# Optimization experiments

Measured on AMD Instinct MI355X. Metric: run time of the kernel, lower is better.

Reference implementation:

```python
import jax, jax.numpy as jnp
import numpy as np

DN = ('NCHW', 'OIHW', 'NCHW')


def conv2d(x, w, pad, dil):
    return jax.lax.conv_general_dilated(x, w, (1, 1), [(pad, pad), (pad, pad)],
                                        rhs_dilation=(dil, dil), dimension_numbers=DN)


def group_norm(x, scale, bias, groups=16, eps=1e-5):
    B, C, H, W = x.shape
    xg = x.reshape(B, groups, -1)
    mu = xg.mean(-1, keepdims=True)
    var = xg.var(-1, keepdims=True)
    xg = (xg - mu) / jnp.sqrt(var + eps)
    return xg.reshape(B, C, H, W) * scale[None, :, None, None] + bias[None, :, None, None]


def aspp_block(x, w, s, b, pad, dil):
    return jax.nn.relu(group_norm(conv2d(x, w, pad, dil), s, b))


def cc_module(q, k, v):
    # criss-cross attention with channel-cosine-normalized q/k
    eps = 1e-10
    qn = q / (jnp.sqrt(jnp.sum(q * q, axis=1, keepdims=True)) + eps)  # norm over channel
    kn = k / (jnp.sqrt(jnp.sum(k * k, axis=1, keepdims=True)) + eps)
    H = q.shape[2]
    # energy along column (vary h') and row (vary w')
    eH = jnp.einsum('bchw,bcgw->bhwg', qn, kn)  # [B,H,W,H]
    eW = jnp.einsum('bchw,bchv->bhwv', qn, kn)  # [B,H,W,W]
    att = jax.nn.softmax(jnp.concatenate([eH, eW], axis=-1), axis=-1)
    attH, attW = att[..., :H], att[..., H:]
    outH = jnp.einsum('bcgw,bhwg->bchw', v, attH)
    outW = jnp.einsum('bchv,bhwv->bchw', v, attW)
    return outH + outW


def cam_module(x, gamma):
    # channel attention with spatial-cosine-normalized similarity
    B, C, H, W = x.shape
    f = x.reshape(B, C, H * W)
    fn = f / (jnp.sqrt(jnp.sum(f * f, axis=-1, keepdims=True)) + 1e-10)
    energy = jnp.einsum('bcn,bdn->bcd', fn, fn)  # [B,C,C]
    att = jax.nn.softmax(energy, axis=-1)
    out = jnp.einsum('bcd,bdn->bcn', att, f).reshape(B, C, H, W)
    return gamma * out + x


def setup_inputs() -> dict:
    key = jax.random.key(0)
    ks = jax.random.split(key, 32)
    C, Cq = 256, 64
    d = {}
    d['x'] = jax.random.normal(ks[0], (4, C, 128, 128), dtype=jnp.float32)
    d['w1'] = jax.random.normal(ks[1], (C, C, 1, 1), jnp.float32) * 0.05
    d['w2'] = jax.random.normal(ks[2], (C, C, 3, 3), jnp.float32) * 0.02
    d['w3'] = jax.random.normal(ks[3], (C, C, 3, 3), jnp.float32) * 0.02
    d['w4'] = jax.random.normal(ks[4], (C, C, 3, 3), jnp.float32) * 0.02
    d['wc'] = jax.random.normal(ks[5], (C, C, 3, 3), jnp.float32) * 0.02
    for i, nm in enumerate(['s1', 's2', 's3', 's4', 'sc']):
        d[nm] = jnp.ones((C,), jnp.float32)
    for nm in ['b1', 'b2', 'b3', 'b4', 'bc']:
        d[nm] = jnp.zeros((C,), jnp.float32)
    d['wq'] = jax.random.normal(ks[6], (Cq, C, 1, 1), jnp.float32) * 0.05
    d['bq'] = jnp.zeros((Cq,), jnp.float32)
    d['wk'] = jax.random.normal(ks[7], (Cq, C, 1, 1), jnp.float32) * 0.05
    d['bk'] = jnp.zeros((Cq,), jnp.float32)
    d['wv'] = jax.random.normal(ks[8], (C, C, 1, 1), jnp.float32) * 0.05
    d['bv'] = jnp.zeros((C,), jnp.float32)
    d['gammas'] = jax.random.normal(ks[9], (5,), jnp.float32) * 0.1
    return d


def reference(x, w1, w2, w3, w4, wc, s1, s2, s3, s4, sc, b1, b2, b3, b4, bc,
              wq, bq, wk, bk, wv, bv, gammas):
    dil = (1, 6, 12, 18)
    x1 = aspp_block(x, w1, s1, b1, pad=0, dil=dil[0])
    x2 = aspp_block(x, w2, s2, b2, pad=dil[1], dil=dil[1])
    x3 = aspp_block(x, w3, s3, b3, pad=dil[2], dil=dil[2])
    x4 = aspp_block(x, w4, s4, b4, pad=dil[3], dil=dil[3])
    x5 = aspp_block(x, wc, sc, bc, pad=1, dil=1)
    for _ in range(2):
        q = conv2d(x5, wq, 0, 1) + bq[None, :, None, None]
        k = conv2d(x5, wk, 0, 1) + bk[None, :, None, None]
        v = conv2d(x5, wv, 0, 1) + bv[None, :, None, None]
        x5 = cc_module(q, k, v)
    L = [x1, x2, x3, x4, x5]
    L = [cam_module(L[i], gammas[i]) for i in range(5)]
    return jnp.stack(L)  # [5, B, C, H, W]
```

## Files before the change

### kernel.cpp

```cpp
#include <hip/hip_runtime.h>
#include <hip/hip_bf16.h>

typedef __hip_bfloat16 bf16;
typedef unsigned short u16;
typedef __attribute__((ext_vector_type(8))) short short8v;
typedef __attribute__((ext_vector_type(4))) float f32x4;

#define BB   4
#define CC_  256
#define HH   128
#define WW   128
#define HWn  16384
#define SZ   ((size_t)16777216)

__device__ __forceinline__ float b2f(bf16 v){ return __bfloat162float(v); }
__device__ __forceinline__ bf16  f2b(float v){ return __float2bfloat16(v); }
__device__ __forceinline__ float us2f(u16 u){
  union { unsigned int i; float f; } x; x.i = ((unsigned int)u) << 16; return x.f;
}
__device__ __forceinline__ u16 f2us(float v){
  bf16 h = f2b(v); u16 u; __builtin_memcpy(&u, &h, 2); return u;
}
__device__ __forceinline__ void st4(float* p, float a, float b, float c, float d){
  *(float4*)p = make_float4(a,b,c,d);
}
__device__ __forceinline__ void st4(bf16* p, float a, float b, float c, float d){
  bf16 o[4] = { f2b(a), f2b(b), f2b(c), f2b(d) };
  *(uint2*)p = *(uint2*)o;
}
__device__ __forceinline__ void store1(float* p, float v){ *p = v; }
__device__ __forceinline__ void store1(bf16* p, float v){ *p = f2b(v); }

typedef __attribute__((address_space(1))) const unsigned int u32g;
typedef __attribute__((address_space(3))) unsigned int u32l;
__device__ __forceinline__ void gl16(const void* g, void* l)
{
  u32g* gp = (u32g*)(unsigned long long)(size_t)g;
  u32l* lp = (u32l*)(unsigned int)(size_t)l;
  __builtin_amdgcn_global_load_lds(gp, lp, 16, 0, 0);
}

__global__ __launch_bounds__(256)
void k_xpose(const float* __restrict__ x, bf16* __restrict__ xt)
{
  const int b = blockIdx.x >> 7, h = blockIdx.x & 127;
  __shared__ u16 L[64][132];
  const int tid = threadIdx.x;
  for (int c0 = 0; c0 < 256; c0 += 64) {
    for (int idx = tid; idx < 2048; idx += 256) {
      const int c = idx >> 5, w4 = (idx & 31) * 4;
      const float4 v = *(const float4*)&x[(((size_t)(b*CC_ + c0 + c))*HH + h)*WW + w4];
      L[c][w4]   = f2us(v.x); L[c][w4+1] = f2us(v.y);
      L[c][w4+2] = f2us(v.z); L[c][w4+3] = f2us(v.w);
    }
    __syncthreads();
    for (int idx = tid; idx < 1024; idx += 256) {
      const int w = idx >> 3, cg = (idx & 7) * 8;
      u16 tmp[8];
      #pragma unroll
      for (int j = 0; j < 8; ++j) tmp[j] = L[cg + j][w];
      *(uint4*)&xt[(((size_t)(b*HH + h))*WW + w)*256 + c0 + cg] = *(uint4*)tmp;
    }
    __syncthreads();
  }
}

__global__ __launch_bounds__(256)
void k_xposeb(const bf16* __restrict__ xt, float* __restrict__ x)
{
  const int b = blockIdx.x >> 7, h = blockIdx.x & 127;
  __shared__ u16 L[64][132];
  const int tid = threadIdx.x;
  for (int c0 = 0; c0 < 256; c0 += 64) {
    for (int idx = tid; idx < 1024; idx += 256) {
      const int w = idx >> 3, cg = (idx & 7) * 8;
      u16 t[8];
      *(uint4*)t = *(const uint4*)((const u16*)xt + (((size_t)(b*HH + h))*WW + w)*256 + c0 + cg);
      #pragma unroll
      for (int j = 0; j < 8; ++j) L[cg + j][w] = t[j];
    }
    __syncthreads();
    for (int idx = tid; idx < 2048; idx += 256) {
      const int c = idx >> 5, w4 = (idx & 31) * 4;
      st4(&x[(((size_t)(b*CC_ + c0 + c))*HH + h)*WW + w4],
          us2f(L[c][w4]), us2f(L[c][w4+1]), us2f(L[c][w4+2]), us2f(L[c][w4+3]));
    }
    __syncthreads();
  }
}

__global__ __launch_bounds__(256)
void k_wt(const float* __restrict__ w, bf16* __restrict__ wt, int taps)
{
  const int i = blockIdx.x * 256 + threadIdx.x;
  const int tap = i >> 16, r = i & 65535;
  const int co = r >> 8, ci = r & 255;
  if (tap < taps) wt[i] = f2b(w[(co*256 + ci)*taps + tap]);
}

template<int KHW, typename DT, bool TRANS>
__global__ __launch_bounds__(256)
void k_convm(const bf16* __restrict__ xt, const bf16* __restrict__ wt,
             const float* __restrict__ bias, DT* __restrict__ dst, int dil, int CO)
{
  const int b   = blockIdx.y >> 7;
  const int h   = blockIdx.y & 127;
  const int co0 = blockIdx.x * 64;
  const int tid = threadIdx.x;
  const int wid = tid >> 6;
  const int lane = tid & 63;
  const int lr = lane & 15;
  const int lg = lane >> 4;
  const int lrow = lane >> 2;
  const int lci  = (lane & 3) * 8;

  __shared__ __align__(16) u16 Asld[KHW*64][32];
  __shared__ __align__(16) u16 Bsld[164][32];

  for (int i = tid; i < 36*32; i += 256) {
    int r = i >> 5; r = (r < 18) ? r : (128 + r);
    Bsld[r][i & 31] = 0;
  }

  f32x4 acc[4][2] = {};

  for (int kh = 0; kh < KHW; ++kh) {
    const int hh = h + (kh - (KHW >> 1)) * dil;
    if (hh < 0 || hh >= HH) continue;
    const bf16* __restrict__ brow = xt + ((size_t)(b*HH + hh))*WW*256;
    for (int kc = 0; kc < 256; kc += 32) {
      for (int ch = wid; ch < KHW*4; ch += 4) {
        const int row = ch*16 + lrow;
        const int tap = row >> 6, cc = row & 63;
        gl16(wt + ((size_t)(kh*KHW + tap))*CO*256 + (co0 + cc)*256 + kc + lci,
             &Asld[ch*16][0]);
      }
      for (int ch = wid; ch < 8; ch += 4) {
        const int wpos = ch*16 + lrow;
        gl16(brow + (size_t)wpos*256 + kc + lci, &Bsld[18 + ch*16][0]);
      }
      __syncthreads();
      #pragma unroll
      for (int kw = 0; kw < KHW; ++kw) {
        const int pbase = 18 + (kw - (KHW >> 1)) * dil;
        short8v af[4], bfr[2];
        #pragma unroll
        for (int cf = 0; cf < 4; ++cf)
          af[cf] = *(const short8v*)&Asld[kw*64 + cf*16 + lr][lg*8];
        #pragma unroll
        for (int wf = 0; wf < 2; ++wf)
          bfr[wf] = *(const short8v*)&Bsld[pbase + wid*32 + wf*16 + lr][lg*8];
        #pragma unroll
        for (int cf = 0; cf < 4; ++cf)
          #pragma unroll
          for (int wf = 0; wf < 2; ++wf)
            acc[cf][wf] = __builtin_amdgcn_mfma_f32_16x16x32_bf16(
                            af[cf], bfr[wf], acc[cf][wf], 0, 0, 0);
      }
      __syncthreads();
    }
  }
  if constexpr (TRANS) {
    #pragma unroll
    for (int cf = 0; cf < 4; ++cf) {
      float bb[4];
      #pragma unroll
      for (int r = 0; r < 4; ++r)
        bb[r] = bias ? bias[co0 + cf*16 + lg*4 + r] : 0.f;
      #pragma unroll
      for (int wf = 0; wf < 2; ++wf) {
        const int wpix = wid*32 + wf*16 + lr;
        bf16* dr = (bf16*)dst + (((size_t)(b*HH + h))*WW + wpix)*CO + co0 + cf*16 + lg*4;
        bf16 o4[4];
        #pragma unroll
        for (int r = 0; r < 4; ++r) o4[r] = f2b(acc[cf][wf][r] + bb[r]);
        *(uint2*)dr = *(uint2*)o4;
      }
    }
  } else {
    #pragma unroll
    for (int cf = 0; cf < 4; ++cf) {
      #pragma unroll
      for (int r = 0; r < 4; ++r) {
        const int co = co0 + cf*16 + lg*4 + r;
        const float bb = bias ? bias[co] : 0.f;
        DT* drow = dst + (((size_t)(b*CO + co))*HH + h)*WW;
        #pragma unroll
        for (int wf = 0; wf < 2; ++wf)
          store1(drow + wid*32 + wf*16 + lr, acc[cf][wf][r] + bb);
      }
    }
  }
}

__global__ __launch_bounds__(256)
void k_gn_stats16(const bf16* __restrict__ t, float* __restrict__ stats)
{
  const int blk = blockIdx.x;
  const int s = blk & 15, bg = blk >> 4;
  const int b = bg >> 4, g = bg & 15;
  const u16* __restrict__ base = (const u16*)t + ((size_t)(b*CC_ + g*16))*HWn + s*1024;
  float s0 = 0.f, s1 = 0.f;
  for (int c = 0; c < 16; ++c) {
    const ushort4 u = *(const ushort4*)(base + (size_t)c * HWn + threadIdx.x*4);
    const float v0 = us2f(u.x), v1 = us2f(u.y), v2 = us2f(u.z), v3 = us2f(u.w);
    s0 += v0 + v1 + v2 + v3;
    s1 = fmaf(v0,v0, fmaf(v1,v1, fmaf(v2,v2, fmaf(v3,v3, s1))));
  }
  #pragma unroll
  for (int o = 32; o > 0; o >>= 1) { s0 += __shfl_down(s0, o, 64); s1 += __shfl_down(s1, o, 64); }
  __shared__ float sh[8];
  const int wid = threadIdx.x >> 6, lane = threadIdx.x & 63;
  if (lane == 0) { sh[wid*2] = s0; sh[wid*2+1] = s1; }
  __syncthreads();
  if (threadIdx.x == 0) {
    atomicAdd(&stats[bg*2],   sh[0]+sh[2]+sh[4]+sh[6]);
    atomicAdd(&stats[bg*2+1], sh[1]+sh[3]+sh[5]+sh[7]);
  }
}

__global__ __launch_bounds__(256)
void k_gn_apply16(const bf16* __restrict__ t, const float* __restrict__ stats,
                  const float* __restrict__ sc, const float* __restrict__ bi,
                  float* __restrict__ dst)
{
  const size_t e = ((size_t)blockIdx.x * 256 + threadIdx.x) * 4;
  const int c  = (int)((e >> 14) & 255);
  const int bg = (int)(e >> 22) * 16 + (c >> 4);
  const float cnt = 16.f * 16384.f;
  const float mu  = stats[bg*2] / cnt;
  const float var = stats[bg*2+1] / cnt - mu * mu;
  const float rs  = rsqrtf(var + 1e-5f);
  const float a   = rs * sc[c];
  const float bb  = bi[c] - mu * a;
  const ushort4 u = *(const ushort4*)((const u16*)t + e);
  st4(dst + e, fmaxf(us2f(u.x)*a+bb,0.f), fmaxf(us2f(u.y)*a+bb,0.f),
               fmaxf(us2f(u.z)*a+bb,0.f), fmaxf(us2f(u.w)*a+bb,0.f));
}

__global__ __launch_bounds__(256)
void k_gn_applyb(const bf16* __restrict__ t, const float* __restrict__ stats,
                 const float* __restrict__ sc, const float* __restrict__ bi,
                 bf16* __restrict__ dst)
{
  const size_t e = ((size_t)blockIdx.x * 256 + threadIdx.x) * 4;
  const int c  = (int)((e >> 14) & 255);
  const int bg = (int)(e >> 22) * 16 + (c >> 4);
  const float cnt = 16.f * 16384.f;
  const float mu  = stats[bg*2] / cnt;
  const float var = stats[bg*2+1] / cnt - mu * mu;
  const float rs  = rsqrtf(var + 1e-5f);
  const float a   = rs * sc[c];
  const float bb  = bi[c] - mu * a;
  const ushort4 u = *(const ushort4*)((const u16*)t + e);
  st4(dst + e, fmaxf(us2f(u.x)*a+bb,0.f), fmaxf(us2f(u.y)*a+bb,0.f),
               fmaxf(us2f(u.z)*a+bb,0.f), fmaxf(us2f(u.w)*a+bb,0.f));
}

__global__ __launch_bounds__(256)
void k_energym(const bf16* __restrict__ fb, float* __restrict__ energy)
{
  const int b  = blockIdx.z;
  const int c0 = (blockIdx.x >> 1) * 128, d0 = (blockIdx.x & 1) * 128;
  const int k0 = blockIdx.y * 512;
  __shared__ __align__(16) u16 Au[2][128][32];
  __shared__ __align__(16) u16 Bu[2][128][32];
  const int tid = threadIdx.x;
  const int wid = tid >> 6, lane = tid & 63;
  const int lr = lane & 15, lg = lane >> 4;
  const int lrow = lane >> 2, lci = (lane & 3) * 8;
  const int row0w = (wid & 1) * 64, col0w = (wid >> 1) * 64;
  const u16* __restrict__ fbb = (const u16*)fb + (size_t)b * CC_ * HWn;

  f32x4 acc[4][4] = {};

  for (int kc = 0; kc < 512; kc += 64) {
    for (int ci = wid; ci < 16; ci += 4) {
      const int seg = ci >> 3, rq = (ci & 7) * 16;
      const int m = rq + lrow;
      gl16(fbb + (size_t)(c0 + m)*HWn + k0 + kc + seg*32 + lci, &Au[seg][rq][0]);
      gl16(fbb + (size_t)(d0 + m)*HWn + k0 + kc + seg*32 + lci, &Bu[seg][rq][0]);
    }
    __syncthreads();
    #pragma unroll
    for (int ks = 0; ks < 2; ++ks) {
      short8v af[4], bfv[4];
      #pragma unroll
      for (int cf = 0; cf < 4; ++cf)
        af[cf] = *(const short8v*)&Au[ks][row0w + cf*16 + lr][lg*8];
      #pragma unroll
      for (int df = 0; df < 4; ++df)
        bfv[df] = *(const short8v*)&Bu[ks][col0w + df*16 + lr][lg*8];
      #pragma unroll
      for (int cf = 0; cf < 4; ++cf)
        #pragma unroll
        for (int df = 0; df < 4; ++df)
          acc[cf][df] = __builtin_amdgcn_mfma_f32_16x16x32_bf16(
                          af[cf], bfv[df], acc[cf][df], 0, 0, 0);
    }
    __syncthreads();
  }
  #pragma unroll
  for (int cf = 0; cf < 4; ++cf)
    #pragma unroll
    for (int df = 0; df < 4; ++df)
      #pragma unroll
      for (int r = 0; r < 4; ++r) {
        const int row = c0 + row0w + cf*16 + lg*4 + r;
        const int col = d0 + col0w + df*16 + lr;
        atomicAdd(&energy[((size_t)(b*CC_ + row))*CC_ + col], acc[cf][df][r]);
      }
}

__global__ __launch_bounds__(512)
void k_camoutm(const float* __restrict__ catt, const bf16* __restrict__ fb,
               float* __restrict__ fio, const float* __restrict__ gammas, int gi)
{
  const int b  = blockIdx.y;
  const int n0 = blockIdx.x * 128;
  __shared__ u16 Au[256][40];
  __shared__ u16 Bu[128][40];
  const int tid = threadIdx.x;
  const int wid = tid >> 6, lane = tid & 63;
  const int lr = lane & 15, lg = lane >> 4;
  const int row0w = (wid & 3) * 64, col0w = (wid >> 2) * 64;

  f32x4 acc[4][4] = {};

  for (int k0 = 0; k0 < 256; k0 += 32) {
    {
      const int m = tid >> 1, kh = (tid & 1) * 16;
      const float* src = catt + ((size_t)(b*CC_ + m))*CC_ + k0 + kh;
      u16 t[16];
      #pragma unroll
      for (int j = 0; j < 4; ++j) {
        const float4 v = *(const float4*)(src + j*4);
        t[j*4]=f2us(v.x); t[j*4+1]=f2us(v.y); t[j*4+2]=f2us(v.z); t[j*4+3]=f2us(v.w);
      }
      *(uint4*)&Au[m][kh]   = *(uint4*)&t[0];
      *(uint4*)&Au[m][kh+8] = *(uint4*)&t[8];
    }
    {
      const int kk = tid >> 4, cl = tid & 15;
      const u16* src = (const u16*)fb + ((size_t)(b*CC_ + k0 + kk))*HWn + n0 + cl;
      #pragma unroll
      for (int j = 0; j < 8; ++j)
        Bu[cl + 16*j][kk] = src[16*j];
    }
    __syncthreads();
    short8v af[4], bfv[4];
    #pragma unroll
    for (int cf = 0; cf < 4; ++cf)
      af[cf] = *(const short8v*)&Au[row0w + cf*16 + lr][lg*8];
    #pragma unroll
    for (int df = 0; df < 4; ++df)
      bfv[df] = *(const short8v*)&Bu[col0w + df*16 + lr][lg*8];
    #pragma unroll
    for (int cf = 0; cf < 4; ++cf)
      #pragma unroll
      for (int df = 0; df < 4; ++df)
        acc[cf][df] = __builtin_amdgcn_mfma_f32_16x16x32_bf16(
                        af[cf], bfv[df], acc[cf][df], 0, 0, 0);
    __syncthreads();
  }
  const float g = gammas[gi];
  #pragma unroll
  for (int cf = 0; cf < 4; ++cf)
    #pragma unroll
    for (int df = 0; df < 4; ++df)
      #pragma unroll
      for (int r = 0; r < 4; ++r) {
        const int row = row0w + cf*16 + lg*4 + r;
        const int col = n0 + col0w + df*16 + lr;
        const size_t o = ((size_t)(b*CC_ + row))*HWn + col;
        fio[o] = g*acc[cf][df][r] + us2f(((const u16*)fb)[o]);
      }
}

__global__ __launch_bounds__(256)
void k_qknorm_t(bf16* __restrict__ q)
{
  const int pix = blockIdx.x * 256 + threadIdx.x;
  u16* __restrict__ base = (u16*)q + (size_t)pix * 64;
  u16 t[64];
  #pragma unroll
  for (int j = 0; j < 8; ++j) *(uint4*)&t[j*8] = *(const uint4*)(base + j*8);
  float s = 0.f;
  #pragma unroll
  for (int c = 0; c < 64; ++c) { const float v = us2f(t[c]); s = fmaf(v, v, s); }
  const float rn = 1.f / (sqrtf(s) + 1e-10f);
  #pragma unroll
  for (int c = 0; c < 64; ++c) t[c] = f2us(us2f(t[c]) * rn);
  #pragma unroll
  for (int j = 0; j < 8; ++j) *(uint4*)(base + j*8) = *(uint4*)&t[j*8];
}

__global__ __launch_bounds__(256)
void k_attHm(const bf16* __restrict__ qt, const bf16* __restrict__ kt,
             bf16* __restrict__ att)
{
  const int b = blockIdx.x >> 7, w = blockIdx.x & 127;
  __shared__ __align__(16) u16 Qs[2][128][32];
  __shared__ __align__(16) u16 Ks[2][128][32];
  const int tid = threadIdx.x;
  const int wid = tid >> 6, lane = tid & 63;
  const int lr = lane & 15, lg = lane >> 4;
  const int lrow = lane >> 2, lci = (lane & 3) * 8;
  const int h0w = (wid & 1) * 64, g0w = (wid >> 1) * 64;
  for (int ci = wid; ci < 16; ci += 4) {
    const int seg = ci >> 3, rq = (ci & 7) * 16;
    const int row = rq + lrow;
    const size_t gb = (((size_t)(b*HH + row))*WW + w)*64 + seg*32 + lci;
    gl16((const u16*)qt + gb, &Qs[seg][rq][0]);
    gl16((const u16*)kt + gb, &Ks[seg][rq][0]);
  }
  __syncthreads();
  f32x4 acc[4][4] = {};
  #pragma unroll
  for (int ks = 0; ks < 2; ++ks) {
    short8v af[4], bfv[4];
    #pragma unroll
    for (int hf = 0; hf < 4; ++hf)
      af[hf] = *(const short8v*)&Qs[ks][h0w + hf*16 + lr][lg*8];
    #pragma unroll
    for (int gf = 0; gf < 4; ++gf)
      bfv[gf] = *(const short8v*)&Ks[ks][g0w + gf*16 + lr][lg*8];
    #pragma unroll
    for (int hf = 0; hf < 4; ++hf)
      #pragma unroll
      for (int gf = 0; gf < 4; ++gf)
        acc[hf][gf] = __builtin_amdgcn_mfma_f32_16x16x32_bf16(
                        af[hf], bfv[gf], acc[hf][gf], 0, 0, 0);
  }
  #pragma unroll
  for (int hf = 0; hf < 4; ++hf)
    #pragma unroll
    for (int r = 0; r < 4; ++r) {
      const int h = h0w + hf*16 + lg*4 + r;
      u16* prow = (u16*)att + (((size_t)b*HH + h)*WW + w)*256 + g0w;
      #pragma unroll
      for (int gf = 0; gf < 4; ++gf)
        prow[gf*16 + lr] = f2us(acc[hf][gf][r]);
    }
}

__global__ __launch_bounds__(256)
void k_attWm(const bf16* __restrict__ qt, const bf16* __restrict__ kt,
             bf16* __restrict__ att)
{
  const int b = blockIdx.x >> 7, h = blockIdx.x & 127;
  __shared__ __align__(16) u16 Qs[2][128][32];
  __shared__ __align__(16) u16 Ks[2][128][32];
  const int tid = threadIdx.x;
  const int wid = tid >> 6, lane = tid & 63;
  const int lr = lane & 15, lg = lane >> 4;
  const int lrow = lane >> 2, lci = (lane & 3) * 8;
  const int w0w = (wid & 1) * 64, v0w = (wid >> 1) * 64;
  for (int ci = wid; ci < 16; ci += 4) {
    const int seg = ci >> 3, rq = (ci & 7) * 16;
    const int row = rq + lrow;
    const size_t gb = (((size_t)(b*HH + h))*WW + row)*64 + seg*32 + lci;
    gl16((const u16*)qt + gb, &Qs[seg][rq][0]);
    gl16((const u16*)kt + gb, &Ks[seg][rq][0]);
  }
  __syncthreads();
  f32x4 acc[4][4] = {};
  #pragma unroll
  for (int ks = 0; ks < 2; ++ks) {
    short8v af[4], bfv[4];
    #pragma unroll
    for (int wf = 0; wf < 4; ++wf)
      af[wf] = *(const short8v*)&Qs[ks][w0w + wf*16 + lr][lg*8];
    #pragma unroll
    for (int vf = 0; vf < 4; ++vf)
      bfv[vf] = *(const short8v*)&Ks[ks][v0w + vf*16 + lr][lg*8];
    #pragma unroll
    for (int wf = 0; wf < 4; ++wf)
      #pragma unroll
      for (int vf = 0; vf < 4; ++vf)
        acc[wf][vf] = __builtin_amdgcn_mfma_f32_16x16x32_bf16(
                        af[wf], bfv[vf], acc[wf][vf], 0, 0, 0);
  }
  #pragma unroll
  for (int wf = 0; wf < 4; ++wf)
    #pragma unroll
    for (int r = 0; r < 4; ++r) {
      const int wloc = w0w + wf*16 + lg*4 + r;
      u16* prow = (u16*)att + ((((size_t)b*HH + h)*WW + wloc)*256 + 128) + v0w;
      #pragma unroll
      for (int vf = 0; vf < 4; ++vf)
        prow[vf*16 + lr] = f2us(acc[wf][vf][r]);
    }
}

__global__ __launch_bounds__(256)
void k_ccsm(bf16* __restrict__ att)
{
  const int row  = blockIdx.x * 4 + (threadIdx.x >> 6);
  const int lane = threadIdx.x & 63;
  u16* __restrict__ p = (u16*)att + (size_t)row * 256 + lane * 4;
  const ushort4 u = *(const ushort4*)p;
  float v0 = us2f(u.x), v1 = us2f(u.y), v2 = us2f(u.z), v3 = us2f(u.w);
  float m = fmaxf(fmaxf(v0, v1), fmaxf(v2, v3));
  #pragma unroll
  for (int o = 32; o; o >>= 1) m = fmaxf(m, __shfl_xor(m, o, 64));
  const float e0 = __expf(v0-m), e1 = __expf(v1-m), e2 = __expf(v2-m), e3 = __expf(v3-m);
  float s = e0 + e1 + e2 + e3;
  #pragma unroll
  for (int o = 32; o; o >>= 1) s += __shfl_xor(s, o, 64);
  const float inv = 1.f / s;
  st4((bf16*)p, e0*inv, e1*inv, e2*inv, e3*inv);
}

__global__ __launch_bounds__(256)
void k_outWm(const bf16* __restrict__ vt, const bf16* __restrict__ att,
             bf16* __restrict__ yt)
{
  const int b = blockIdx.y >> 7, h = blockIdx.y & 127;
  const int ch0 = blockIdx.x * 128;
  __shared__ u16 As[128][72];
  __shared__ u16 Bs[128][72];
  const int tid = threadIdx.x;
  const int wid = tid >> 6, lane = tid & 63;
  const int lr = lane & 15, lg = lane >> 4;
  const int w0w = (wid & 1) * 64, c0w = (wid >> 1) * 64;

  f32x4 acc[4][4] = {};

  for (int v0 = 0; v0 < 128; v0 += 64) {
    {
      const int row = tid >> 1, kq = (tid & 1) * 32;
      const u16* src = (const u16*)att + ((((size_t)b*HH + h)*WW + row)*256 + 128) + v0 + kq;
      #pragma unroll
      for (int j = 0; j < 4; ++j)
        *(uint4*)&As[row][kq + j*8] = *(const uint4*)(src + j*8);
    }
    {
      const int vv = tid & 63, cg0 = (tid >> 6) * 32;
      #pragma unroll
      for (int j2 = 0; j2 < 4; ++j2) {
        const int c8 = cg0 + j2*8;
        u16 t[8];
        *(uint4*)t = *(const uint4*)((const u16*)vt +
            (((size_t)(b*HH + h))*WW + (v0 + vv))*256 + ch0 + c8);
        #pragma unroll
        for (int jj = 0; jj < 8; ++jj) Bs[c8 + jj][vv] = t[jj];
      }
    }
    __syncthreads();
    #pragma unroll
    for (int ks = 0; ks < 2; ++ks) {
      short8v af[4], bfv[4];
      #pragma unroll
      for (int wf = 0; wf < 4; ++wf)
        af[wf] = *(const short8v*)&As[w0w + wf*16 + lr][ks*32 + lg*8];
      #pragma unroll
      for (int cf = 0; cf < 4; ++cf)
        bfv[cf] = *(const short8v*)&Bs[c0w + cf*16 + lr][ks*32 + lg*8];
      #pragma unroll
      for (int wf = 0; wf < 4; ++wf)
        #pragma unroll
        for (int cf = 0; cf < 4; ++cf)
          acc[wf][cf] = __builtin_amdgcn_mfma_f32_16x16x32_bf16(
                          af[wf], bfv[cf], acc[wf][cf], 0, 0, 0);
    }
    __syncthreads();
  }
  #pragma unroll
  for (int wf = 0; wf < 4; ++wf)
    #pragma unroll
    for (int r = 0; r < 4; ++r) {
      const int wpix = w0w + wf*16 + lg*4 + r;
      u16* drow = (u16*)yt + (((size_t)(b*HH + h))*WW + wpix)*256 + ch0 + c0w;
      #pragma unroll
      for (int cf = 0; cf < 4; ++cf)
        drow[cf*16 + lr] = f2us(acc[wf][cf][r]);
    }
}

__global__ __launch_bounds__(256)
void k_outHm(const bf16* __restrict__ vt, const bf16* __restrict__ att,
             const bf16* __restrict__ yt, bf16* __restrict__ xt)
{
  const int b = blockIdx.y >> 7, w = blockIdx.y & 127;
  const int ch0 = blockIdx.x * 128;
  __shared__ u16 As[128][72];
  __shared__ u16 Bs[128][72];
  const int tid = threadIdx.x;
  const int wid = tid >> 6, lane = tid & 63;
  const int lr = lane & 15, lg = lane >> 4;
  const int h0w = (wid & 1) * 64, c0w = (wid >> 1) * 64;

  f32x4 acc[4][4] = {};

  for (int g0 = 0; g0 < 128; g0 += 64) {
    {
      const int row = tid >> 1, kq = (tid & 1) * 32;
      const u16* src = (const u16*)att + (((size_t)b*HH + row)*WW + w)*256 + g0 + kq;
      #pragma unroll
      for (int j = 0; j < 4; ++j)
        *(uint4*)&As[row][kq + j*8] = *(const uint4*)(src + j*8);
    }
    {
      const int gg = tid & 63, cg0 = (tid >> 6) * 32;
      #pragma unroll
      for (int j2 = 0; j2 < 4; ++j2) {
        const int c8 = cg0 + j2*8;
        u16 t[8];
        *(uint4*)t = *(const uint4*)((const u16*)vt +
            (((size_t)(b*HH + (g0 + gg)))*WW + w)*256 + ch0 + c8);
        #pragma unroll
        for (int jj = 0; jj < 8; ++jj) Bs[c8 + jj][gg] = t[jj];
      }
    }
    __syncthreads();
    #pragma unroll
    for (int ks = 0; ks < 2; ++ks) {
      short8v af[4], bfv[4];
      #pragma unroll
      for (int hf = 0; hf < 4; ++hf)
        af[hf] = *(const short8v*)&As[h0w + hf*16 + lr][ks*32 + lg*8];
      #pragma unroll
      for (int cf = 0; cf < 4; ++cf)
        bfv[cf] = *(const short8v*)&Bs[c0w + cf*16 + lr][ks*32 + lg*8];
      #pragma unroll
      for (int hf = 0; hf < 4; ++hf)
        #pragma unroll
        for (int cf = 0; cf < 4; ++cf)
          acc[hf][cf] = __builtin_amdgcn_mfma_f32_16x16x32_bf16(
                          af[hf], bfv[cf], acc[hf][cf], 0, 0, 0);
    }
    __syncthreads();
  }
  #pragma unroll
  for (int hf = 0; hf < 4; ++hf)
    #pragma unroll
    for (int r = 0; r < 4; ++r) {
      const int hh = h0w + hf*16 + lg*4 + r;
      const size_t base = (((size_t)(b*HH + hh))*WW + w)*256 + ch0 + c0w;
      #pragma unroll
      for (int cf = 0; cf < 4; ++cf) {
        const size_t o = base + cf*16 + lr;
        ((u16*)xt)[o] = f2us(acc[hf][cf][r] + us2f(((const u16*)yt)[o]));
      }
    }
}

__global__ __launch_bounds__(256)
void k_rownb(const float* __restrict__ f, bf16* __restrict__ fb,
             float* __restrict__ rown)
{
  const int bc = blockIdx.x;
  const float* __restrict__ p = f + (size_t)bc * HWn;
  u16* __restrict__ ob = (u16*)fb + (size_t)bc * HWn;
  float s = 0.f;
  for (int i = threadIdx.x * 8; i < HWn; i += 2048) {
    const float4 a = *(const float4*)(p + i);
    const float4 b4 = *(const float4*)(p + i + 4);
    u16 t[8] = { f2us(a.x), f2us(a.y), f2us(a.z), f2us(a.w),
                 f2us(b4.x), f2us(b4.y), f2us(b4.z), f2us(b4.w) };
    *(uint4*)(ob + i) = *(uint4*)t;
    s = fmaf(a.x,a.x, fmaf(a.y,a.y, fmaf(a.z,a.z, fmaf(a.w,a.w, s))));
    s = fmaf(b4.x,b4.x, fmaf(b4.y,b4.y, fmaf(b4.z,b4.z, fmaf(b4.w,b4.w, s))));
  }
  #pragma unroll
  for (int o = 32; o > 0; o >>= 1) s += __shfl_down(s, o, 64);
  __shared__ float sh[4];
  const int wid = threadIdx.x >> 6, lane = threadIdx.x & 63;
  if (lane == 0) sh[wid] = s;
  __syncthreads();
  if (threadIdx.x == 0) rown[bc] = sqrtf(sh[0]+sh[1]+sh[2]+sh[3]) + 1e-10f;
}

__global__ __launch_bounds__(256)
void k_rown16(const bf16* __restrict__ fb, float* __restrict__ rown)
{
  const int bc = blockIdx.x;
  const u16* __restrict__ p = (const u16*)fb + (size_t)bc * HWn;
  float s = 0.f;
  for (int i = threadIdx.x * 8; i < HWn; i += 2048) {
    u16 t[8];
    *(uint4*)t = *(const uint4*)(p + i);
    #pragma unroll
    for (int j = 0; j < 8; ++j) { const float v = us2f(t[j]); s = fmaf(v, v, s); }
  }
  #pragma unroll
  for (int o = 32; o > 0; o >>= 1) s += __shfl_down(s, o, 64);
  __shared__ float sh[4];
  const int wid = threadIdx.x >> 6, lane = threadIdx.x & 63;
  if (lane == 0) sh[wid] = s;
  __syncthreads();
  if (threadIdx.x == 0) rown[bc] = sqrtf(sh[0]+sh[1]+sh[2]+sh[3]) + 1e-10f;
}

__global__ __launch_bounds__(256)
void k_camsm(float* __restrict__ energy, const float* __restrict__ rown)
{
  const int row  = blockIdx.x * 4 + (threadIdx.x >> 6);
  const int lane = threadIdx.x & 63;
  const int b = row >> 8;
  float* __restrict__ p = energy + (size_t)row * 256 + lane * 4;
  const float rc = rown[row];
  const float4 rd = *(const float4*)(rown + b*256 + lane*4);
  float4 v = *(const float4*)p;
  v.x /= (rc*rd.x); v.y /= (rc*rd.y); v.z /= (rc*rd.z); v.w /= (rc*rd.w);
  float m = fmaxf(fmaxf(v.x, v.y), fmaxf(v.z, v.w));
  #pragma unroll
  for (int o = 32; o; o >>= 1) m = fmaxf(m, __shfl_xor(m, o, 64));
  const float e0 = __expf(v.x-m), e1 = __expf(v.y-m), e2 = __expf(v.z-m), e3 = __expf(v.w-m);
  float s = e0 + e1 + e2 + e3;
  #pragma unroll
  for (int o = 32; o; o >>= 1) s += __shfl_xor(s, o, 64);
  const float inv = 1.f / s;
  *(float4*)p = make_float4(e0*inv, e1*inv, e2*inv, e3*inv);
}

extern "C" void kernel_launch(void* const* d_in, const int* in_sizes, int n_in,
                              void* d_out, int out_size, void* d_ws, size_t ws_size,
                              hipStream_t stream)
{
  const float* x     = (const float*)d_in[0];
  const float* w_[5]  = {(const float*)d_in[1],(const float*)d_in[2],(const float*)d_in[3],(const float*)d_in[4],(const float*)d_in[5]};
  const float* s_[5]  = {(const float*)d_in[6],(const float*)d_in[7],(const float*)d_in[8],(const float*)d_in[9],(const float*)d_in[10]};
  const float* bi_[5] = {(const float*)d_in[11],(const float*)d_in[12],(const float*)d_in[13],(const float*)d_in[14],(const float*)d_in[15]};
  const float* wq = (const float*)d_in[16];
  const float* bq = (const float*)d_in[17];
  const float* wk = (const float*)d_in[18];
  const float* bk = (const float*)d_in[19];
  const float* wv = (const float*)d_in[20];
  const float* bv = (const float*)d_in[21];
  const float* gam = (const float*)d_in[22];
  float* out = (float*)d_out;

  char* wsc = (char*)d_ws;
  bf16*  Tc16 = (bf16*)wsc;
  bf16*  qt   = (bf16*)wsc;
  bf16*  kt   = qt + SZ/4;
  bf16*  vt   = qt + SZ/2;
  bf16*  attb = qt + SZ/2 + SZ;
  bf16*  xt   = attb + SZ;
  bf16*  yt   = xt + SZ;
  bf16*  wtb  = yt + SZ;
  bf16*  wtq  = wtb;
  bf16*  wtk  = wtb + 16384;
  bf16*  wtv  = wtb + 32768;
  float* stats  = (float*)(wtb + 16*65536);
  float* energy = stats + 128;
  float* rown   = energy + 262144;
  float* slot4 = out + 4*SZ;
  bf16*  fbA   = attb;
  bf16*  fb16  = vt;

  const int dil_[5] = {1, 6, 12, 18, 1};

  k_xpose<<<512,256,0,stream>>>(x, xt);
  for (int i = 0; i < 4; ++i) {
    hipMemsetAsync(stats, 0, 128*sizeof(float), stream);
    const int taps = (i == 0) ? 1 : 9;
    k_wt<<<taps*256,256,0,stream>>>(w_[i], wtb, taps);
    if (i == 0) k_convm<1,bf16,false><<<dim3(4,512),256,0,stream>>>(xt, wtb, nullptr, Tc16, 1, 256);
    else        k_convm<3,bf16,false><<<dim3(4,512),256,0,stream>>>(xt, wtb, nullptr, Tc16, dil_[i], 256);
    k_gn_stats16<<<1024,256,0,stream>>>(Tc16, stats);
    k_gn_applyb<<<16384,256,0,stream>>>(Tc16, stats, s_[i], bi_[i], fbA);
    hipMemsetAsync(energy, 0, 262144*sizeof(float), stream);
    k_rown16<<<1024,256,0,stream>>>(fbA, rown);
    k_energym<<<dim3(4,32,4),256,0,stream>>>(fbA, energy);
    k_camsm<<<256,256,0,stream>>>(energy, rown);
    k_camoutm<<<dim3(128,4),512,0,stream>>>(energy, fbA, out + (size_t)i*SZ, gam, i);
  }

  {
    hipMemsetAsync(stats, 0, 128*sizeof(float), stream);
    k_wt<<<9*256,256,0,stream>>>(w_[4], wtb, 9);
    k_convm<3,bf16,false><<<dim3(4,512),256,0,stream>>>(xt, wtb, nullptr, Tc16, 1, 256);
    k_gn_stats16<<<1024,256,0,stream>>>(Tc16, stats);
    k_gn_apply16<<<16384,256,0,stream>>>(Tc16, stats, s_[4], bi_[4], slot4);
  }

  k_wt<<<64,256,0,stream>>>(wq, wtq, 1);
  k_wt<<<64,256,0,stream>>>(wk, wtk, 1);
  k_wt<<<256,256,0,stream>>>(wv, wtv, 1);
  k_xpose<<<512,256,0,stream>>>(slot4, xt);
  for (int it = 0; it < 2; ++it) {
    k_convm<1,bf16,true><<<dim3(1,512),256,0,stream>>>(xt, wtq, bq, qt, 1, 64);
    k_convm<1,bf16,true><<<dim3(1,512),256,0,stream>>>(xt, wtk, bk, kt, 1, 64);
    k_convm<1,bf16,true><<<dim3(4,512),256,0,stream>>>(xt, wtv, bv, vt, 1, 256);
    k_qknorm_t<<<256,256,0,stream>>>(qt);
    k_qknorm_t<<<256,256,0,stream>>>(kt);
    k_attHm<<<512,256,0,stream>>>(qt, kt, attb);
    k_attWm<<<512,256,0,stream>>>(qt, kt, attb);
    k_ccsm<<<16384,256,0,stream>>>(attb);
    k_outWm<<<dim3(2,512),256,0,stream>>>(vt, attb, yt);
    k_outHm<<<dim3(2,512),256,0,stream>>>(vt, attb, yt, xt);
  }
  k_xposeb<<<512,256,0,stream>>>(xt, slot4);

  {
    hipMemsetAsync(energy, 0, 262144*sizeof(float), stream);
    k_rownb<<<1024,256,0,stream>>>(slot4, fb16, rown);
    k_energym<<<dim3(4,32,4),256,0,stream>>>(fb16, energy);
    k_camsm<<<256,256,0,stream>>>(energy, rown);
    k_camoutm<<<dim3(128,4),512,0,stream>>>(energy, fb16, slot4, gam, 4);
  }
}
```

Before: 1.340 ms.

## Fuse GroupNorm stats into conv epilogue and CAM row norms into GN apply

The conv epilogue now accumulates per-group sum and sum-of-squares of the bf16-rounded outputs and adds them atomically, which removes the separate GN stats kernel. The bf16 GN apply also accumulates per-channel squared norms for the CAM normalization, removing the k_rown16 pass in the four ASPP branches; the square root moves into the softmax kernel, and one memset now zeroes stats, energy and row norms together. The final transpose writes bf16 directly for the last CAM, skipping the fp32 round trip through slot4. In exchange it adds atomics and a block reduction in the conv epilogue, which may raise register pressure.

```diff
diff --git a/kernel.cpp b/kernel.cpp
--- a/kernel.cpp
+++ b/kernel.cpp
@@ -66,7 +66,7 @@
 }
 
 __global__ __launch_bounds__(256)
-void k_xposeb(const bf16* __restrict__ xt, float* __restrict__ x)
+void k_xposeb_b(const bf16* __restrict__ xt, bf16* __restrict__ fb)
 {
   const int b = blockIdx.x >> 7, h = blockIdx.x & 127;
   __shared__ u16 L[64][132];
@@ -82,8 +82,8 @@
     __syncthreads();
     for (int idx = tid; idx < 2048; idx += 256) {
       const int c = idx >> 5, w4 = (idx & 31) * 4;
-      st4(&x[(((size_t)(b*CC_ + c0 + c))*HH + h)*WW + w4],
-          us2f(L[c][w4]), us2f(L[c][w4+1]), us2f(L[c][w4+2]), us2f(L[c][w4+3]));
+      u16 q[4] = { L[c][w4], L[c][w4+1], L[c][w4+2], L[c][w4+3] };
+      *(uint2*)((u16*)fb + (((size_t)(b*CC_ + c0 + c))*HH + h)*WW + w4) = *(uint2*)q;
     }
     __syncthreads();
   }
@@ -98,10 +98,11 @@
   if (tap < taps) wt[i] = f2b(w[(co*256 + ci)*taps + tap]);
 }
 
-template<int KHW, typename DT, bool TRANS>
+template<int KHW, typename DT, bool TRANS, bool STATS>
 __global__ __launch_bounds__(256)
 void k_convm(const bf16* __restrict__ xt, const bf16* __restrict__ wt,
-             const float* __restrict__ bias, DT* __restrict__ dst, int dil, int CO)
+             const float* __restrict__ bias, DT* __restrict__ dst, int dil, int CO,
+             float* __restrict__ stats)
 {
   const int b   = blockIdx.y >> 7;
   const int h   = blockIdx.y & 127;
@@ -178,6 +179,7 @@
       }
     }
   } else {
+    float s0[4] = {0.f,0.f,0.f,0.f}, s1[4] = {0.f,0.f,0.f,0.f};
     #pragma unroll
     for (int cf = 0; cf < 4; ++cf) {
       #pragma unroll
@@ -186,36 +188,37 @@
         const float bb = bias ? bias[co] : 0.f;
         DT* drow = dst + (((size_t)(b*CO + co))*HH + h)*WW;
         #pragma unroll
-        for (int wf = 0; wf < 2; ++wf)
-          store1(drow + wid*32 + wf*16 + lr, acc[cf][wf][r] + bb);
-      }
-    }
-  }
-}
-
-__global__ __launch_bounds__(256)
-void k_gn_stats16(const bf16* __restrict__ t, float* __restrict__ stats)
-{
-  const int blk = blockIdx.x;
-  const int s = blk & 15, bg = blk >> 4;
-  const int b = bg >> 4, g = bg & 15;
-  const u16* __restrict__ base = (const u16*)t + ((size_t)(b*CC_ + g*16))*HWn + s*1024;
-  float s0 = 0.f, s1 = 0.f;
-  for (int c = 0; c < 16; ++c) {
-    const ushort4 u = *(const ushort4*)(base + (size_t)c * HWn + threadIdx.x*4);
-    const float v0 = us2f(u.x), v1 = us2f(u.y), v2 = us2f(u.z), v3 = us2f(u.w);
-    s0 += v0 + v1 + v2 + v3;
-    s1 = fmaf(v0,v0, fmaf(v1,v1, fmaf(v2,v2, fmaf(v3,v3, s1))));
-  }
-  #pragma unroll
-  for (int o = 32; o > 0; o >>= 1) { s0 += __shfl_down(s0, o, 64); s1 += __shfl_down(s1, o, 64); }
-  __shared__ float sh[8];
-  const int wid = threadIdx.x >> 6, lane = threadIdx.x & 63;
-  if (lane == 0) { sh[wid*2] = s0; sh[wid*2+1] = s1; }
-  __syncthreads();
-  if (threadIdx.x == 0) {
-    atomicAdd(&stats[bg*2],   sh[0]+sh[2]+sh[4]+sh[6]);
-    atomicAdd(&stats[bg*2+1], sh[1]+sh[3]+sh[5]+sh[7]);
+        for (int wf = 0; wf < 2; ++wf) {
+          const float v = acc[cf][wf][r] + bb;
+          store1(drow + wid*32 + wf*16 + lr, v);
+          if constexpr (STATS) {
+            const float vr = us2f(f2us(v));
+            s0[cf] += vr;
+            s1[cf] = fmaf(vr, vr, s1[cf]);
+          }
+        }
+      }
+    }
+    if constexpr (STATS) {
+      #pragma unroll
+      for (int cf = 0; cf < 4; ++cf)
+        #pragma unroll
+        for (int o = 32; o > 0; o >>= 1) {
+          s0[cf] += __shfl_down(s0[cf], o, 64);
+          s1[cf] += __shfl_down(s1[cf], o, 64);
+        }
+      __shared__ float sred[4][4][2];
+      if (lane == 0) {
+        #pragma unroll
+        for (int cf = 0; cf < 4; ++cf) { sred[wid][cf][0] = s0[cf]; sred[wid][cf][1] = s1[cf]; }
+      }
+      __syncthreads();
+      if (tid < 8) {
+        const int cf = tid >> 1, j = tid & 1;
+        const float t = sred[0][cf][j] + sred[1][cf][j] + sred[2][cf][j] + sred[3][cf][j];
+        atomicAdd(&stats[(b*16 + (co0 >> 4) + cf)*2 + j], t);
+      }
+    }
   }
 }
 
@@ -241,7 +244,7 @@
 __global__ __launch_bounds__(256)
 void k_gn_applyb(const bf16* __restrict__ t, const float* __restrict__ stats,
                  const float* __restrict__ sc, const float* __restrict__ bi,
-                 bf16* __restrict__ dst)
+                 bf16* __restrict__ dst, float* __restrict__ rownsq)
 {
   const size_t e = ((size_t)blockIdx.x * 256 + threadIdx.x) * 4;
   const int c  = (int)((e >> 14) & 255);
@@ -253,8 +256,19 @@
   const float a   = rs * sc[c];
   const float bb  = bi[c] - mu * a;
   const ushort4 u = *(const ushort4*)((const u16*)t + e);
-  st4(dst + e, fmaxf(us2f(u.x)*a+bb,0.f), fmaxf(us2f(u.y)*a+bb,0.f),
-               fmaxf(us2f(u.z)*a+bb,0.f), fmaxf(us2f(u.w)*a+bb,0.f));
+  u16 q[4] = { f2us(fmaxf(us2f(u.x)*a+bb,0.f)), f2us(fmaxf(us2f(u.y)*a+bb,0.f)),
+               f2us(fmaxf(us2f(u.z)*a+bb,0.f)), f2us(fmaxf(us2f(u.w)*a+bb,0.f)) };
+  *(uint2*)((u16*)dst + e) = *(uint2*)q;
+  float sq = 0.f;
+  #pragma unroll
+  for (int j = 0; j < 4; ++j) { const float w = us2f(q[j]); sq = fmaf(w, w, sq); }
+  #pragma unroll
+  for (int o = 32; o > 0; o >>= 1) sq += __shfl_down(sq, o, 64);
+  __shared__ float sh[4];
+  const int wid = threadIdx.x >> 6, lane = threadIdx.x & 63;
+  if (lane == 0) sh[wid] = sq;
+  __syncthreads();
+  if (threadIdx.x == 0) atomicAdd(&rownsq[blockIdx.x >> 4], sh[0]+sh[1]+sh[2]+sh[3]);
 }
 
 __global__ __launch_bounds__(256)
@@ -647,32 +661,6 @@
 }
 
 __global__ __launch_bounds__(256)
-void k_rownb(const float* __restrict__ f, bf16* __restrict__ fb,
-             float* __restrict__ rown)
-{
-  const int bc = blockIdx.x;
-  const float* __restrict__ p = f + (size_t)bc * HWn;
-  u16* __restrict__ ob = (u16*)fb + (size_t)bc * HWn;
-  float s = 0.f;
-  for (int i = threadIdx.x * 8; i < HWn; i += 2048) {
-    const float4 a = *(const float4*)(p + i);
-    const float4 b4 = *(const float4*)(p + i + 4);
-    u16 t[8] = { f2us(a.x), f2us(a.y), f2us(a.z), f2us(a.w),
-                 f2us(b4.x), f2us(b4.y), f2us(b4.z), f2us(b4.w) };
-    *(uint4*)(ob + i) = *(uint4*)t;
-    s = fmaf(a.x,a.x, fmaf(a.y,a.y, fmaf(a.z,a.z, fmaf(a.w,a.w, s))));
-    s = fmaf(b4.x,b4.x, fmaf(b4.y,b4.y, fmaf(b4.z,b4.z, fmaf(b4.w,b4.w, s))));
-  }
-  #pragma unroll
-  for (int o = 32; o > 0; o >>= 1) s += __shfl_down(s, o, 64);
-  __shared__ float sh[4];
-  const int wid = threadIdx.x >> 6, lane = threadIdx.x & 63;
-  if (lane == 0) sh[wid] = s;
-  __syncthreads();
-  if (threadIdx.x == 0) rown[bc] = sqrtf(sh[0]+sh[1]+sh[2]+sh[3]) + 1e-10f;
-}
-
-__global__ __launch_bounds__(256)
 void k_rown16(const bf16* __restrict__ fb, float* __restrict__ rown)
 {
   const int bc = blockIdx.x;
@@ -690,7 +678,7 @@
   const int wid = threadIdx.x >> 6, lane = threadIdx.x & 63;
   if (lane == 0) sh[wid] = s;
   __syncthreads();
-  if (threadIdx.x == 0) rown[bc] = sqrtf(sh[0]+sh[1]+sh[2]+sh[3]) + 1e-10f;
+  if (threadIdx.x == 0) rown[bc] = sh[0]+sh[1]+sh[2]+sh[3];
 }
 
 __global__ __launch_bounds__(256)
@@ -700,8 +688,10 @@
   const int lane = threadIdx.x & 63;
   const int b = row >> 8;
   float* __restrict__ p = energy + (size_t)row * 256 + lane * 4;
-  const float rc = rown[row];
-  const float4 rd = *(const float4*)(rown + b*256 + lane*4);
+  const float rc = sqrtf(rown[row]) + 1e-10f;
+  float4 rd = *(const float4*)(rown + b*256 + lane*4);
+  rd.x = sqrtf(rd.x) + 1e-10f; rd.y = sqrtf(rd.y) + 1e-10f;
+  rd.z = sqrtf(rd.z) + 1e-10f; rd.w = sqrtf(rd.w) + 1e-10f;
   float4 v = *(const float4*)p;
   v.x /= (rc*rd.x); v.y /= (rc*rd.y); v.z /= (rc*rd.z); v.w /= (rc*rd.w);
   float m = fmaxf(fmaxf(v.x, v.y), fmaxf(v.z, v.w));
@@ -755,15 +745,12 @@
 
   k_xpose<<<512,256,0,stream>>>(x, xt);
   for (int i = 0; i < 4; ++i) {
-    hipMemsetAsync(stats, 0, 128*sizeof(float), stream);
+    hipMemsetAsync(stats, 0, (size_t)(128 + 262144 + 1024)*sizeof(float), stream);
     const int taps = (i == 0) ? 1 : 9;
     k_wt<<<taps*256,256,0,stream>>>(w_[i], wtb, taps);
-    if (i == 0) k_convm<1,bf16,false><<<dim3(4,512),256,0,stream>>>(xt, wtb, nullptr, Tc16, 1, 256);
-    else        k_convm<3,bf16,false><<<dim3(4,512),256,0,stream>>>(xt, wtb, nullptr, Tc16, dil_[i], 256);
-    k_gn_stats16<<<1024,256,0,stream>>>(Tc16, stats);
-    k_gn_applyb<<<16384,256,0,stream>>>(Tc16, stats, s_[i], bi_[i], fbA);
-    hipMemsetAsync(energy, 0, 262144*sizeof(float), stream);
-    k_rown16<<<1024,256,0,stream>>>(fbA, rown);
+    if (i == 0) k_convm<1,bf16,false,true><<<dim3(4,512),256,0,stream>>>(xt, wtb, nullptr, Tc16, 1, 256, stats);
+    else        k_convm<3,bf16,false,true><<<dim3(4,512),256,0,stream>>>(xt, wtb, nullptr, Tc16, dil_[i], 256, stats);
+    k_gn_applyb<<<16384,256,0,stream>>>(Tc16, stats, s_[i], bi_[i], fbA, rown);
     k_energym<<<dim3(4,32,4),256,0,stream>>>(fbA, energy);
     k_camsm<<<256,256,0,stream>>>(energy, rown);
     k_camoutm<<<dim3(128,4),512,0,stream>>>(energy, fbA, out + (size_t)i*SZ, gam, i);
@@ -772,8 +759,7 @@
   {
     hipMemsetAsync(stats, 0, 128*sizeof(float), stream);
     k_wt<<<9*256,256,0,stream>>>(w_[4], wtb, 9);
-    k_convm<3,bf16,false><<<dim3(4,512),256,0,stream>>>(xt, wtb, nullptr, Tc16, 1, 256);
-    k_gn_stats16<<<1024,256,0,stream>>>(Tc16, stats);
+    k_convm<3,bf16,false,true><<<dim3(4,512),256,0,stream>>>(xt, wtb, nullptr, Tc16, 1, 256, stats);
     k_gn_apply16<<<16384,256,0,stream>>>(Tc16, stats, s_[4], bi_[4], slot4);
   }
 
@@ -782,9 +768,9 @@
   k_wt<<<256,256,0,stream>>>(wv, wtv, 1);
   k_xpose<<<512,256,0,stream>>>(slot4, xt);
   for (int it = 0; it < 2; ++it) {
-    k_convm<1,bf16,true><<<dim3(1,512),256,0,stream>>>(xt, wtq, bq, qt, 1, 64);
-    k_convm<1,bf16,true><<<dim3(1,512),256,0,stream>>>(xt, wtk, bk, kt, 1, 64);
-    k_convm<1,bf16,true><<<dim3(4,512),256,0,stream>>>(xt, wtv, bv, vt, 1, 256);
+    k_convm<1,bf16,true,false><<<dim3(1,512),256,0,stream>>>(xt, wtq, bq, qt, 1, 64, nullptr);
+    k_convm<1,bf16,true,false><<<dim3(1,512),256,0,stream>>>(xt, wtk, bk, kt, 1, 64, nullptr);
+    k_convm<1,bf16,true,false><<<dim3(4,512),256,0,stream>>>(xt, wtv, bv, vt, 1, 256, nullptr);
     k_qknorm_t<<<256,256,0,stream>>>(qt);
     k_qknorm_t<<<256,256,0,stream>>>(kt);
     k_attHm<<<512,256,0,stream>>>(qt, kt, attb);
@@ -793,11 +779,11 @@
     k_outWm<<<dim3(2,512),256,0,stream>>>(vt, attb, yt);
     k_outHm<<<dim3(2,512),256,0,stream>>>(vt, attb, yt, xt);
   }
-  k_xposeb<<<512,256,0,stream>>>(xt, slot4);
 
   {
+    k_xposeb_b<<<512,256,0,stream>>>(xt, fb16);
     hipMemsetAsync(energy, 0, 262144*sizeof(float), stream);
-    k_rownb<<<1024,256,0,stream>>>(slot4, fb16, rown);
+    k_rown16<<<1024,256,0,stream>>>(fb16, rown);
     k_energym<<<dim3(4,32,4),256,0,stream>>>(fb16, energy);
     k_camsm<<<256,256,0,stream>>>(energy, rown);
     k_camoutm<<<dim3(128,4),512,0,stream>>>(energy, fb16, slot4, gam, 4);
```

Result: faster. 1.310 ms (-2.3%).
